# Performance work log

Hardware: AMD Instinct MI355X
Metric: run time of the kernel (lower is better)

Reference implementation:

```python
import jax, jax.numpy as jnp
import numpy as np

B, S, D = 2, 2048, 1024
H, HD = 16, 64  # num_heads, head_dim; H*HD == D


def setup_inputs() -> dict:
    key = jax.random.key(0)
    ks = jax.random.split(key, 5)
    scale = 1.0 / np.sqrt(D)
    return {
        "inputs": jax.random.normal(ks[0], (B, S, D), jnp.float32),
        "Wq": jax.random.normal(ks[1], (D, H * HD), jnp.float32) * scale,
        "bq": jnp.zeros((H * HD,), jnp.float32),
        "Wk": jax.random.normal(ks[2], (D, H * HD), jnp.float32) * scale,
        "bk": jnp.zeros((H * HD,), jnp.float32),
        "Wv": jax.random.normal(ks[3], (D, H * HD), jnp.float32) * scale,
        "bv": jnp.zeros((H * HD,), jnp.float32),
        "Wo": jax.random.normal(ks[4], (H * HD, D), jnp.float32) * scale,
        "bo": jnp.zeros((D,), jnp.float32),
    }


def reference(inputs, Wq, bq, Wk, bk, Wv, bv, Wo, bo):
    b, s, _ = inputs.shape
    # QKV projections, split into heads: [b, s, H, HD]
    q = (inputs @ Wq + bq).reshape(b, s, H, HD)
    k = (inputs @ Wk + bk).reshape(b, s, H, HD)
    v = (inputs @ Wv + bv).reshape(b, s, H, HD)
    # scaled dot-product attention (non-causal, full)
    scores = jnp.einsum('bqhd,bkhd->bhqk', q, k) / jnp.sqrt(jnp.float32(HD))
    attn = jax.nn.softmax(scores, axis=-1)
    out = jnp.einsum('bhql,blhd->bqhd', attn, v).reshape(b, s, H * HD)
    return out @ Wo + bo
```

## Files before the change

kernel.cpp:

```cpp
#include <hip/hip_runtime.h>
#include <hip/hip_bf16.h>

typedef __attribute__((ext_vector_type(8))) _Float16 half8;
typedef __attribute__((ext_vector_type(4))) _Float16 half4;
typedef __attribute__((ext_vector_type(2))) _Float16 half2v;
typedef __attribute__((ext_vector_type(4))) __fp16 fp16x4;
typedef __attribute__((ext_vector_type(4))) float f32x4;

#define MFMA16(a, b, c) __builtin_amdgcn_mfma_f32_16x16x32_f16(a, b, c, 0, 0, 0)
#define MFMA16K16(a, b, c)                                                         \
    __builtin_amdgcn_mfma_f32_16x16x16f16(__builtin_bit_cast(fp16x4, a),           \
                                          __builtin_bit_cast(fp16x4, b), c, 0, 0, 0)

typedef const __attribute__((address_space(1))) unsigned int GU32;
typedef __attribute__((address_space(3))) unsigned int LU32;

__device__ __forceinline__ void async_copy16(const _Float16* g, _Float16* l) {
    __builtin_amdgcn_global_load_lds((GU32*)g, (LU32*)l, 16, 0, 0);
}

__device__ __forceinline__ half2v pack2(float a, float b) {
    return __builtin_bit_cast(half2v, __builtin_amdgcn_cvt_pkrtz(a, b));
}

#define QSCALE 0.18033688011112042f

__global__ __launch_bounds__(256) void prep(
    const float* __restrict__ X, _Float16* __restrict__ Xh,
    const float* __restrict__ W0, const float* __restrict__ W1,
    const float* __restrict__ W2, const float* __restrict__ W3,
    _Float16* __restrict__ T0, _Float16* __restrict__ T1,
    _Float16* __restrict__ T2, _Float16* __restrict__ T3) {
    __shared__ float t[32][33];
    const int bid = blockIdx.x, tid = threadIdx.x;
    if (bid < 4096) {
        int i = (bid * 256 + tid) * 4;
        float4 v = *(const float4*)(X + i);
        half4 o = {(_Float16)v.x, (_Float16)v.y, (_Float16)v.z, (_Float16)v.w};
        *(half4*)(Xh + i) = o;
    } else {
        const int bid2 = bid - 4096;
        const int z = bid2 >> 10, tt = bid2 & 1023;
        const int bx = tt & 31, by = tt >> 5;
        const int tx = tid & 31, ty = tid >> 5;
        const float* src = z == 0 ? W0 : z == 1 ? W1 : z == 2 ? W2 : W3;
        _Float16* dst    = z == 0 ? T0 : z == 1 ? T1 : z == 2 ? T2 : T3;
        const int x = bx * 32 + tx;
        const int y0 = by * 32;
        for (int i = ty; i < 32; i += 8)
            t[i][tx] = src[(size_t)(y0 + i) * 1024 + x];
        __syncthreads();
        const int nx = y0 + tx;
        const int ny = bx * 32;
        for (int i = ty; i < 32; i += 8)
            dst[(size_t)(ny + i) * 1024 + nx] = (_Float16)t[tx][i];
    }
}

__global__ __launch_bounds__(256) void qkv_gemm(
    const _Float16* __restrict__ Xh,
    const _Float16* __restrict__ WTq, const _Float16* __restrict__ WTk,
    const _Float16* __restrict__ WTv,
    const float* __restrict__ bq, const float* __restrict__ bk,
    const float* __restrict__ bv,
    _Float16* __restrict__ Qo, _Float16* __restrict__ Ko,
    _Float16* __restrict__ Vto) {
    __shared__ __attribute__((aligned(16))) _Float16 Als[128 * 32];
    __shared__ __attribute__((aligned(16))) _Float16 Bls[128 * 32];

    const int wsel = blockIdx.y >> 3;
    const _Float16* WT = wsel == 0 ? WTq : wsel == 1 ? WTk : WTv;
    const float* bias  = wsel == 0 ? bq  : wsel == 1 ? bk  : bv;

    const int tid = threadIdx.x, w = tid >> 6, lane = tid & 63;
    const int quad = lane >> 4, l16 = lane & 15;
    const int wr = (w >> 1) * 64, wc = (w & 1) * 64;
    const int mBase = blockIdx.x * 128, nBase = (blockIdx.y & 7) * 128;
    const _Float16* Ab = Xh + (size_t)mBase * 1024;
    const _Float16* Bb = WT + (size_t)nBase * 1024;

    f32x4 acc[4][4] = {};

    for (int k0 = 0; k0 < 1024; k0 += 32) {
        __syncthreads();
#pragma unroll
        for (int iss = 0; iss < 2; ++iss) {
            int u = iss * 256 + tid;
            int r = u >> 2, c8 = (u & 3) * 8;
            _Float16* lA = Als + (size_t)(iss * 256 + (tid & 192)) * 8;
            _Float16* lB = Bls + (size_t)(iss * 256 + (tid & 192)) * 8;
            async_copy16(Ab + (size_t)r * 1024 + k0 + c8, lA);
            async_copy16(Bb + (size_t)r * 1024 + k0 + c8, lB);
        }
        __syncthreads();
        half8 af[4], bfr[4];
#pragma unroll
        for (int i = 0; i < 4; ++i) af[i]  = ((const half8*)Als)[(wr + i * 16 + l16) * 4 + quad];
#pragma unroll
        for (int j = 0; j < 4; ++j) bfr[j] = ((const half8*)Bls)[(wc + j * 16 + l16) * 4 + quad];
#pragma unroll
        for (int i = 0; i < 4; ++i)
#pragma unroll
            for (int j = 0; j < 4; ++j) acc[i][j] = MFMA16(af[i], bfr[j], acc[i][j]);
    }

    const float scale = (wsel == 0) ? QSCALE : 1.0f;
#pragma unroll
    for (int i = 0; i < 4; ++i) {
        const int row = mBase + wr + i * 16 + quad * 4;
#pragma unroll
        for (int j = 0; j < 4; ++j) {
            const int col = nBase + wc + j * 16 + l16;
            const float bb = bias[col];
            const int hh = col >> 6, hd = col & 63;
            if (wsel == 2) {
                const int bi = row >> 11, s = row & 2047;
                half4 pv;
#pragma unroll
                for (int r = 0; r < 4; ++r) pv[r] = (_Float16)((acc[i][j][r] + bb) * scale);
                *(half4*)(Vto + ((size_t)(bi * 16 + hh) * 64 + hd) * 2048 + s) = pv;
            } else {
                _Float16* dst = (wsel == 0) ? Qo : Ko;
#pragma unroll
                for (int r = 0; r < 4; ++r) {
                    const int token = row + r;
                    const int bi = token >> 11, s = token & 2047;
                    dst[((size_t)(bi * 16 + hh) * 2048 + s) * 64 + hd] =
                        (_Float16)((acc[i][j][r] + bb) * scale);
                }
            }
        }
    }
}

__global__ __launch_bounds__(256) void attn_kernel(
    const _Float16* __restrict__ Q, const _Float16* __restrict__ K,
    const _Float16* __restrict__ Vt, _Float16* __restrict__ O) {
    const int bh = blockIdx.y;
    const int b = bh >> 4, h = bh & 15;
    const int qt = blockIdx.x;
    const int tid = threadIdx.x, w = tid >> 6, lane = tid & 63;
    const int quad = lane >> 4, l16 = lane & 15;

    __shared__ __attribute__((aligned(16))) _Float16 Kls[2][4096];
    __shared__ __attribute__((aligned(16))) _Float16 Vls[2][4096];

    const _Float16* Qb = Q  + (size_t)bh * 2048 * 64;
    const _Float16* Kb = K  + (size_t)bh * 2048 * 64;
    const _Float16* Vb = Vt + (size_t)bh * 64 * 2048;

    const int u0 = tid, u1 = 256 + tid;
    const int r0 = u0 >> 3, c0 = (u0 & 7) ^ (r0 & 7);
    const int r1 = u1 >> 3, c1 = (u1 & 7) ^ (r1 & 7);
    const int lbase0 = (tid & 192) * 8;
    const int lbase1 = 2048 + (tid & 192) * 8;

    half8 qf[2][2];
#pragma unroll
    for (int g = 0; g < 2; ++g) {
        const int q = qt * 128 + w * 32 + g * 16 + l16;
#pragma unroll
        for (int kc = 0; kc < 2; ++kc)
            qf[g][kc] = *(const half8*)(Qb + (size_t)q * 64 + kc * 32 + quad * 8);
    }

    f32x4 oacc[2][4] = {};
    float l[2] = {0.f, 0.f};

    {
        async_copy16(Kb + (size_t)r0 * 64 + c0 * 8, (_Float16*)Kls[0] + lbase0);
        async_copy16(Kb + (size_t)r1 * 64 + c1 * 8, (_Float16*)Kls[0] + lbase1);
        async_copy16(Vb + (size_t)r0 * 2048 + c0 * 8, (_Float16*)Vls[0] + lbase0);
        async_copy16(Vb + (size_t)r1 * 2048 + c1 * 8, (_Float16*)Vls[0] + lbase1);
    }

    const int sw = l16 & 7;
    for (int kt = 0; kt < 32; ++kt) {
        __syncthreads();
        const _Float16* Kc = Kls[kt & 1];
        const _Float16* Vc = Vls[kt & 1];
        if (kt + 1 < 32) {
            const int nb = (kt + 1) * 64;
            _Float16* kd = (_Float16*)Kls[(kt + 1) & 1];
            _Float16* vd = (_Float16*)Vls[(kt + 1) & 1];
            async_copy16(Kb + (size_t)(nb + r0) * 64 + c0 * 8, kd + lbase0);
            async_copy16(Kb + (size_t)(nb + r1) * 64 + c1 * 8, kd + lbase1);
            async_copy16(Vb + (size_t)r0 * 2048 + nb + c0 * 8, vd + lbase0);
            async_copy16(Vb + (size_t)r1 * 2048 + nb + c1 * 8, vd + lbase1);
        }
        f32x4 s0[4] = {}, s1[4] = {};
#pragma unroll
        for (int nt = 0; nt < 4; ++nt) {
            const int key = nt * 16 + l16;
            half8 k0 = *(const half8*)(Kc + ((size_t)key * 8 + (quad ^ sw)) * 8);
            half8 k1 = *(const half8*)(Kc + ((size_t)key * 8 + ((4 + quad) ^ sw)) * 8);
            s0[nt] = MFMA16(k0, qf[0][0], s0[nt]);
            s0[nt] = MFMA16(k1, qf[0][1], s0[nt]);
            s1[nt] = MFMA16(k0, qf[1][0], s1[nt]);
            s1[nt] = MFMA16(k1, qf[1][1], s1[nt]);
        }
        half4 pB[2][4];
#pragma unroll
        for (int g = 0; g < 2; ++g) {
            f32x4* s = g ? s1 : s0;
#pragma unroll
            for (int nt = 0; nt < 4; ++nt) {
                float p0 = __builtin_amdgcn_exp2f(s[nt][0]);
                float p1 = __builtin_amdgcn_exp2f(s[nt][1]);
                float p2 = __builtin_amdgcn_exp2f(s[nt][2]);
                float p3 = __builtin_amdgcn_exp2f(s[nt][3]);
                l[g] += (p0 + p1) + (p2 + p3);
                ((half2v*)&pB[g][nt])[0] = pack2(p0, p1);
                ((half2v*)&pB[g][nt])[1] = pack2(p2, p3);
            }
        }
#pragma unroll
        for (int nt = 0; nt < 4; ++nt) {
            const int chunk = (nt << 1) + (quad >> 1);
#pragma unroll
            for (int j = 0; j < 4; ++j) {
                const int hd = j * 16 + l16;
                half4 vf = *(const half4*)(Vc + ((size_t)hd * 8 + (chunk ^ sw)) * 8 +
                                           (quad & 1) * 4);
                oacc[0][j] = MFMA16K16(vf, pB[0][nt], oacc[0][j]);
                oacc[1][j] = MFMA16K16(vf, pB[1][nt], oacc[1][j]);
            }
        }
    }
#pragma unroll
    for (int g = 0; g < 2; ++g) {
        float lt = l[g];
        lt += __shfl_xor(lt, 16);
        lt += __shfl_xor(lt, 32);
        const float inv = __builtin_amdgcn_rcpf(lt);
        const int token = b * 2048 + qt * 128 + w * 32 + g * 16 + l16;
#pragma unroll
        for (int j = 0; j < 4; ++j) {
            half4 ov;
#pragma unroll
            for (int r = 0; r < 4; ++r) ov[r] = (_Float16)(oacc[g][j][r] * inv);
            *(half4*)&O[(size_t)token * 1024 + h * 64 + j * 16 + quad * 4] = ov;
        }
    }
}

__global__ __launch_bounds__(256) void out_gemm(
    const _Float16* __restrict__ Oh, const _Float16* __restrict__ WTo,
    const float* __restrict__ bo, float* __restrict__ Y) {
    __shared__ __attribute__((aligned(16))) _Float16 Als[64 * 32];
    __shared__ __attribute__((aligned(16))) _Float16 Bls[128 * 32];
    const int tid = threadIdx.x, w = tid >> 6, lane = tid & 63;
    const int quad = lane >> 4, l16 = lane & 15;
    const int wr = (w >> 1) * 32, wc = (w & 1) * 64;
    const int mBase = blockIdx.x * 64, nBase = blockIdx.y * 128;
    const _Float16* Ab = Oh + (size_t)mBase * 1024;
    const _Float16* Bb = WTo + (size_t)nBase * 1024;

    f32x4 acc[2][4] = {};
    for (int k0 = 0; k0 < 1024; k0 += 32) {
        __syncthreads();
        {
            int r = tid >> 2, c8 = (tid & 3) * 8;
            _Float16* lA = Als + (size_t)(tid & 192) * 8;
            async_copy16(Ab + (size_t)r * 1024 + k0 + c8, lA);
        }
#pragma unroll
        for (int iss = 0; iss < 2; ++iss) {
            int u = iss * 256 + tid;
            int r = u >> 2, c8 = (u & 3) * 8;
            _Float16* lB = Bls + (size_t)(iss * 256 + (tid & 192)) * 8;
            async_copy16(Bb + (size_t)r * 1024 + k0 + c8, lB);
        }
        __syncthreads();
        half8 af[2], bfr[4];
#pragma unroll
        for (int i = 0; i < 2; ++i) af[i]  = ((const half8*)Als)[(wr + i * 16 + l16) * 4 + quad];
#pragma unroll
        for (int j = 0; j < 4; ++j) bfr[j] = ((const half8*)Bls)[(wc + j * 16 + l16) * 4 + quad];
#pragma unroll
        for (int i = 0; i < 2; ++i)
#pragma unroll
            for (int j = 0; j < 4; ++j) acc[i][j] = MFMA16(af[i], bfr[j], acc[i][j]);
    }
#pragma unroll
    for (int i = 0; i < 2; ++i) {
        const int row = mBase + wr + i * 16 + quad * 4;
#pragma unroll
        for (int j = 0; j < 4; ++j) {
            const int col = nBase + wc + j * 16 + l16;
            const float bb = bo[col];
#pragma unroll
            for (int r = 0; r < 4; ++r)
                Y[(size_t)(row + r) * 1024 + col] = acc[i][j][r] + bb;
        }
    }
}

extern "C" void kernel_launch(void* const* d_in, const int* in_sizes, int n_in,
                              void* d_out, int out_size, void* d_ws, size_t ws_size,
                              hipStream_t stream) {
    const float* X  = (const float*)d_in[0];
    const float* Wq = (const float*)d_in[1];
    const float* bq = (const float*)d_in[2];
    const float* Wk = (const float*)d_in[3];
    const float* bk = (const float*)d_in[4];
    const float* Wv = (const float*)d_in[5];
    const float* bv = (const float*)d_in[6];
    const float* Wo = (const float*)d_in[7];
    const float* bo = (const float*)d_in[8];
    float* Y = (float*)d_out;

    char* ws = (char*)d_ws;
    _Float16* Xh  = (_Float16*)(ws);
    _Float16* WTq = (_Float16*)(ws + (8ull << 20));
    _Float16* WTk = (_Float16*)(ws + (10ull << 20));
    _Float16* WTv = (_Float16*)(ws + (12ull << 20));
    _Float16* WTo = (_Float16*)(ws + (14ull << 20));
    _Float16* Qh  = (_Float16*)(ws + (16ull << 20));
    _Float16* Kh  = (_Float16*)(ws + (24ull << 20));
    _Float16* Vth = (_Float16*)(ws + (32ull << 20));
    _Float16* Oh  = (_Float16*)(ws + (40ull << 20));

    prep<<<8192, 256, 0, stream>>>(X, Xh, Wq, Wk, Wv, Wo, WTq, WTk, WTv, WTo);
    qkv_gemm<<<dim3(32, 24), 256, 0, stream>>>(Xh, WTq, WTk, WTv, bq, bk, bv, Qh, Kh, Vth);
    attn_kernel<<<dim3(16, 32), 256, 0, stream>>>(Qh, Kh, Vth, Oh);
    out_gemm<<<dim3(64, 8), 256, 0, stream>>>(Oh, WTo, bo, Y);
}
```

Before: 214.8 us.

## Split attention key range across two wave groups with LDS reduction

The attention kernel now runs 512 threads per block. Two groups of four waves each handle alternating 64-key tiles for the same 128 queries, so each group does 16 iterations instead of 32. The partial outputs and row sums are combined through shared memory at the end. This raises waves per block and shortens the serial key loop, which should help latency hiding. The cost is double the LDS footprint (64KB), an extra reduction step, and possibly lower block occupancy per CU.

```diff
diff --git a/kernel.cpp b/kernel.cpp
--- a/kernel.cpp
+++ b/kernel.cpp
@@ -133,7 +133,7 @@
     }
 }
 
-__global__ __launch_bounds__(256) void attn_kernel(
+__global__ __launch_bounds__(512) void attn_kernel(
     const _Float16* __restrict__ Q, const _Float16* __restrict__ K,
     const _Float16* __restrict__ Vt, _Float16* __restrict__ O) {
     const int bh = blockIdx.y;
@@ -141,24 +141,27 @@
     const int qt = blockIdx.x;
     const int tid = threadIdx.x, w = tid >> 6, lane = tid & 63;
     const int quad = lane >> 4, l16 = lane & 15;
-
-    __shared__ __attribute__((aligned(16))) _Float16 Kls[2][4096];
-    __shared__ __attribute__((aligned(16))) _Float16 Vls[2][4096];
+    const int ws2 = w & 3, stream = w >> 2;
+
+    __shared__ __attribute__((aligned(16))) _Float16 smem[32768];
+    _Float16 (*Kls)[2][4096] = (_Float16(*)[2][4096])smem;
+    _Float16 (*Vls)[2][4096] = (_Float16(*)[2][4096])(smem + 16384);
 
     const _Float16* Qb = Q  + (size_t)bh * 2048 * 64;
     const _Float16* Kb = K  + (size_t)bh * 2048 * 64;
     const _Float16* Vb = Vt + (size_t)bh * 64 * 2048;
 
-    const int u0 = tid, u1 = 256 + tid;
+    const int stid = tid & 255, sgrp = tid >> 8;
+    const int u0 = stid, u1 = 256 + stid;
     const int r0 = u0 >> 3, c0 = (u0 & 7) ^ (r0 & 7);
     const int r1 = u1 >> 3, c1 = (u1 & 7) ^ (r1 & 7);
-    const int lbase0 = (tid & 192) * 8;
-    const int lbase1 = 2048 + (tid & 192) * 8;
+    const int lbase0 = (stid & 192) * 8;
+    const int lbase1 = 2048 + (stid & 192) * 8;
 
     half8 qf[2][2];
 #pragma unroll
     for (int g = 0; g < 2; ++g) {
-        const int q = qt * 128 + w * 32 + g * 16 + l16;
+        const int q = qt * 128 + ws2 * 32 + g * 16 + l16;
 #pragma unroll
         for (int kc = 0; kc < 2; ++kc)
             qf[g][kc] = *(const half8*)(Qb + (size_t)q * 64 + kc * 32 + quad * 8);
@@ -168,21 +171,24 @@
     float l[2] = {0.f, 0.f};
 
     {
-        async_copy16(Kb + (size_t)r0 * 64 + c0 * 8, (_Float16*)Kls[0] + lbase0);
-        async_copy16(Kb + (size_t)r1 * 64 + c1 * 8, (_Float16*)Kls[0] + lbase1);
-        async_copy16(Vb + (size_t)r0 * 2048 + c0 * 8, (_Float16*)Vls[0] + lbase0);
-        async_copy16(Vb + (size_t)r1 * 2048 + c1 * 8, (_Float16*)Vls[0] + lbase1);
+        const int nb = sgrp * 64;
+        _Float16* kd = &Kls[sgrp][0][0];
+        _Float16* vd = &Vls[sgrp][0][0];
+        async_copy16(Kb + (size_t)(nb + r0) * 64 + c0 * 8, kd + lbase0);
+        async_copy16(Kb + (size_t)(nb + r1) * 64 + c1 * 8, kd + lbase1);
+        async_copy16(Vb + (size_t)r0 * 2048 + nb + c0 * 8, vd + lbase0);
+        async_copy16(Vb + (size_t)r1 * 2048 + nb + c1 * 8, vd + lbase1);
     }
 
     const int sw = l16 & 7;
-    for (int kt = 0; kt < 32; ++kt) {
-        __syncthreads();
-        const _Float16* Kc = Kls[kt & 1];
-        const _Float16* Vc = Vls[kt & 1];
-        if (kt + 1 < 32) {
-            const int nb = (kt + 1) * 64;
-            _Float16* kd = (_Float16*)Kls[(kt + 1) & 1];
-            _Float16* vd = (_Float16*)Vls[(kt + 1) & 1];
+    for (int it = 0; it < 16; ++it) {
+        __syncthreads();
+        const _Float16* Kc = &Kls[stream][it & 1][0];
+        const _Float16* Vc = &Vls[stream][it & 1][0];
+        if (it + 1 < 16) {
+            const int nb = (2 * (it + 1) + sgrp) * 64;
+            _Float16* kd = &Kls[sgrp][(it + 1) & 1][0];
+            _Float16* vd = &Vls[sgrp][(it + 1) & 1][0];
             async_copy16(Kb + (size_t)(nb + r0) * 64 + c0 * 8, kd + lbase0);
             async_copy16(Kb + (size_t)(nb + r1) * 64 + c1 * 8, kd + lbase1);
             async_copy16(Vb + (size_t)r0 * 2048 + nb + c0 * 8, vd + lbase0);
@@ -227,19 +233,41 @@
             }
         }
     }
-#pragma unroll
-    for (int g = 0; g < 2; ++g) {
-        float lt = l[g];
-        lt += __shfl_xor(lt, 16);
-        lt += __shfl_xor(lt, 32);
-        const float inv = __builtin_amdgcn_rcpf(lt);
-        const int token = b * 2048 + qt * 128 + w * 32 + g * 16 + l16;
-#pragma unroll
-        for (int j = 0; j < 4; ++j) {
-            half4 ov;
-#pragma unroll
-            for (int r = 0; r < 4; ++r) ov[r] = (_Float16)(oacc[g][j][r] * inv);
-            *(half4*)&O[(size_t)token * 1024 + h * 64 + j * 16 + quad * 4] = ov;
+    __syncthreads();
+    float* red  = (float*)smem;
+    float* redl = (float*)smem + 4 * 64 * 36;
+    const int rb = (ws2 * 64 + lane) * 36;
+    if (stream == 1) {
+#pragma unroll
+        for (int g = 0; g < 2; ++g) {
+#pragma unroll
+            for (int j = 0; j < 4; ++j)
+                *(f32x4*)&red[rb + (g * 4 + j) * 4] = oacc[g][j];
+            redl[(ws2 * 64 + lane) * 2 + g] = l[g];
+        }
+    }
+    __syncthreads();
+    if (stream == 0) {
+#pragma unroll
+        for (int g = 0; g < 2; ++g) {
+#pragma unroll
+            for (int j = 0; j < 4; ++j) {
+                f32x4 o2 = *(const f32x4*)&red[rb + (g * 4 + j) * 4];
+#pragma unroll
+                for (int r = 0; r < 4; ++r) oacc[g][j][r] += o2[r];
+            }
+            float lt = l[g] + redl[(ws2 * 64 + lane) * 2 + g];
+            lt += __shfl_xor(lt, 16);
+            lt += __shfl_xor(lt, 32);
+            const float inv = __builtin_amdgcn_rcpf(lt);
+            const int token = b * 2048 + qt * 128 + ws2 * 32 + g * 16 + l16;
+#pragma unroll
+            for (int j = 0; j < 4; ++j) {
+                half4 ov;
+#pragma unroll
+                for (int r = 0; r < 4; ++r) ov[r] = (_Float16)(oacc[g][j][r] * inv);
+                *(half4*)&O[(size_t)token * 1024 + h * 64 + j * 16 + quad * 4] = ov;
+            }
         }
     }
 }
@@ -323,6 +351,6 @@
 
     prep<<<8192, 256, 0, stream>>>(X, Xh, Wq, Wk, Wv, Wo, WTq, WTk, WTv, WTo);
     qkv_gemm<<<dim3(32, 24), 256, 0, stream>>>(Xh, WTq, WTk, WTv, bq, bk, bv, Qh, Kh, Vth);
-    attn_kernel<<<dim3(16, 32), 256, 0, stream>>>(Qh, Kh, Vth, Oh);
+    attn_kernel<<<dim3(16, 32), 512, 0, stream>>>(Qh, Kh, Vth, Oh);
     out_gemm<<<dim3(64, 8), 256, 0, stream>>>(Oh, WTo, bo, Y);
 }
```

Result: faster. 200.5 us (-6.7%).
